# Performance work log

Measured on AMD Instinct MI355X. Metric: run time of the kernel, lower is better.

Reference implementation:

```python
import jax, jax.numpy as jnp
import numpy as np

B, L, C = 8, 3136, 192
HEADS, HEAD_CH = 3, 64
EPS = 1e-5


def _dwconv(x, w, s):
    # depthwise 3x3 conv, SAME padding; w: [3,3,1,C], feature_group_count=C
    return jax.lax.conv_general_dilated(
        x, w, (s, s), 'SAME',
        dimension_numbers=('NHWC', 'HWIO', 'NHWC'),
        feature_group_count=x.shape[-1])


def _proj(x, dw, scale, bias, mean, var, pw, s):
    # depthwise conv -> BN (inference, running stats) -> 1x1 pointwise conv
    h = _dwconv(x, dw, s)
    h = (h - mean) * jax.lax.rsqrt(var + EPS) * scale + bias
    return jax.lax.conv_general_dilated(
        h, pw, (1, 1), 'SAME',
        dimension_numbers=('NHWC', 'HWIO', 'NHWC'))


def setup_inputs() -> dict:
    key = jax.random.key(0)
    ks = jax.random.split(key, 7)
    d = {'x': jax.random.normal(ks[0], (B, L, C), jnp.float32)}
    for i, p in enumerate(['q', 'k', 'v']):
        d[p + '_dw'] = jax.random.normal(ks[i + 1], (3, 3, 1, C), jnp.float32) * 0.1
        d[p + '_scale'] = jnp.ones((C,), jnp.float32)
        d[p + '_bias'] = jnp.zeros((C,), jnp.float32)
        d[p + '_mean'] = jnp.zeros((C,), jnp.float32)
        d[p + '_var'] = jnp.ones((C,), jnp.float32)
        d[p + '_pw'] = jax.random.normal(ks[i + 4], (1, 1, C, HEADS * HEAD_CH), jnp.float32) * 0.05
    d['is_training'] = 0  # inference: BN uses running averages
    return d


def reference(x, q_dw, q_scale, q_bias, q_mean, q_var, q_pw,
              k_dw, k_scale, k_bias, k_mean, k_var, k_pw,
              v_dw, v_scale, v_bias, v_mean, v_var, v_pw,
              is_training):
    S = int(np.ceil(np.sqrt(L)))  # 56; L is a perfect square, so no token padding
    xi = x.reshape(B, S, S, C)
    q = _proj(xi, q_dw, q_scale, q_bias, q_mean, q_var, q_pw, 1)  # [B,56,56,192]
    k = _proj(xi, k_dw, k_scale, k_bias, k_mean, k_var, k_pw, 2)  # [B,28,28,192]
    v = _proj(xi, v_dw, v_scale, v_bias, v_mean, v_var, v_pw, 2)  # [B,28,28,192]
    q = q.reshape(B, -1, HEADS, HEAD_CH) / jnp.sqrt(jnp.float32(HEAD_CH))
    k = k.reshape(B, -1, HEADS, HEAD_CH)
    v = v.reshape(B, -1, HEADS, HEAD_CH)
    attn = jax.nn.softmax(jnp.einsum('bqhd,bkhd->bhqk', q, k), axis=-1)
    o = jnp.einsum('bhqk,bkhd->bqhd', attn, v)
    # num_heads*head_ch == out_ch -> plain head merge, no output projection
    return o.reshape(B, L, HEADS * HEAD_CH)
```

## Files before the change

kernel.cpp:

```cpp
#include <hip/hip_runtime.h>
#include <cmath>

#define EPS_BN 1e-5f

typedef __bf16 bf16;
typedef __bf16 bf16x4 __attribute__((ext_vector_type(4)));
typedef __bf16 bf16x8 __attribute__((ext_vector_type(8)));
typedef float  f32x4  __attribute__((ext_vector_type(4)));

__device__ __forceinline__ void dma16(const bf16* g, bf16* l) {
    __builtin_amdgcn_global_load_lds(
        (const __attribute__((address_space(1))) void*)g,
        (__attribute__((address_space(3))) void*)l, 16, 0, 0);
}

__global__ __launch_bounds__(256) void conv_all_kernel(
    const float* __restrict__ x,
    const float* __restrict__ qdw, const float* __restrict__ qscale,
    const float* __restrict__ qbias, const float* __restrict__ qmean,
    const float* __restrict__ qvar,
    const float* __restrict__ kdw, const float* __restrict__ kscale,
    const float* __restrict__ kbias, const float* __restrict__ kmean,
    const float* __restrict__ kvar,
    const float* __restrict__ vdw, const float* __restrict__ vscale,
    const float* __restrict__ vbias, const float* __restrict__ vmean,
    const float* __restrict__ vvar,
    const float* __restrict__ qpw, const float* __restrict__ kpw,
    const float* __restrict__ vpw,
    bf16* __restrict__ qhi, bf16* __restrict__ qlo,
    bf16* __restrict__ khi, bf16* __restrict__ klo,
    bf16* __restrict__ vhi, bf16* __restrict__ vlo,
    bf16* __restrict__ wt) {
    const int WW = 56, C = 192;
    int bid = blockIdx.x;

    if (bid < 4704) {
        int idx = bid * 256 + threadIdx.x;
        int p  = idx / 48;
        int c4 = (idx - p * 48) * 4;
        int b  = p / 3136;
        int rem = p - b * 3136;
        int oy = rem / 56;
        int ox = rem - oy * 56;
        const float* xb = x + (size_t)b * 3136 * C;

        float4 sc = *(const float4*)&qscale[c4];
        float4 vr = *(const float4*)&qvar[c4];
        float4 bi = *(const float4*)&qbias[c4];
        float4 mn = *(const float4*)&qmean[c4];
        float aA[4] = {sc.x * rsqrtf(vr.x + EPS_BN), sc.y * rsqrtf(vr.y + EPS_BN),
                       sc.z * rsqrtf(vr.z + EPS_BN), sc.w * rsqrtf(vr.w + EPS_BN)};
        float aB[4] = {bi.x - mn.x * aA[0], bi.y - mn.y * aA[1],
                       bi.z - mn.z * aA[2], bi.w - mn.w * aA[3]};
        float s[4] = {0.f, 0.f, 0.f, 0.f};
#pragma unroll
        for (int ky = 0; ky < 3; ky++) {
            int iy = oy + ky - 1;
            bool yok = (iy >= 0) && (iy < 56);
#pragma unroll
            for (int kx = 0; kx < 3; kx++) {
                int ix = ox + kx - 1;
                if (yok && ix >= 0 && ix < WW) {
                    float4 xv = *(const float4*)&xb[((size_t)iy * WW + ix) * C + c4];
                    float4 wv = *(const float4*)&qdw[(ky * 3 + kx) * C + c4];
                    s[0] += xv.x * wv.x; s[1] += xv.y * wv.y;
                    s[2] += xv.z * wv.z; s[3] += xv.w * wv.w;
                }
            }
        }
        bf16x4 hv, lv;
#pragma unroll
        for (int j = 0; j < 4; j++) {
            float av = s[j] * aA[j] + aB[j];
            bf16 hh = (bf16)av;
            hv[j] = hh;
            lv[j] = (bf16)(av - (float)hh);
        }
        *(bf16x4*)&qhi[(size_t)p * C + c4] = hv;
        *(bf16x4*)&qlo[(size_t)p * C + c4] = lv;
    } else if (bid < 5880) {
        int idx = (bid - 4704) * 256 + threadIdx.x;
        int p  = idx / 48;
        int c4 = (idx - p * 48) * 4;
        int b  = p / 784;
        int rem = p - b * 784;
        int oy = rem / 28;
        int ox = rem - oy * 28;
        const float* xb = x + (size_t)b * 3136 * C;

        float ks[4] = {0.f, 0.f, 0.f, 0.f};
        float vs[4] = {0.f, 0.f, 0.f, 0.f};
#pragma unroll
        for (int ky = 0; ky < 3; ky++) {
            int iy = oy * 2 + ky;
            bool yok = iy < 56;
#pragma unroll
            for (int kx = 0; kx < 3; kx++) {
                int ix = ox * 2 + kx;
                if (yok && ix < WW) {
                    float4 xv = *(const float4*)&xb[((size_t)iy * WW + ix) * C + c4];
                    float4 kw = *(const float4*)&kdw[(ky * 3 + kx) * C + c4];
                    float4 vw = *(const float4*)&vdw[(ky * 3 + kx) * C + c4];
                    ks[0] += xv.x * kw.x; ks[1] += xv.y * kw.y;
                    ks[2] += xv.z * kw.z; ks[3] += xv.w * kw.w;
                    vs[0] += xv.x * vw.x; vs[1] += xv.y * vw.y;
                    vs[2] += xv.z * vw.z; vs[3] += xv.w * vw.w;
                }
            }
        }
        float4 ksc = *(const float4*)&kscale[c4];
        float4 kvr = *(const float4*)&kvar[c4];
        float4 kbi = *(const float4*)&kbias[c4];
        float4 kmn = *(const float4*)&kmean[c4];
        float4 vsc = *(const float4*)&vscale[c4];
        float4 vvr = *(const float4*)&vvar[c4];
        float4 vbi = *(const float4*)&vbias[c4];
        float4 vmn = *(const float4*)&vmean[c4];
        float kA[4] = {ksc.x * rsqrtf(kvr.x + EPS_BN), ksc.y * rsqrtf(kvr.y + EPS_BN),
                       ksc.z * rsqrtf(kvr.z + EPS_BN), ksc.w * rsqrtf(kvr.w + EPS_BN)};
        float kB[4] = {kbi.x - kmn.x * kA[0], kbi.y - kmn.y * kA[1],
                       kbi.z - kmn.z * kA[2], kbi.w - kmn.w * kA[3]};
        float vA[4] = {vsc.x * rsqrtf(vvr.x + EPS_BN), vsc.y * rsqrtf(vvr.y + EPS_BN),
                       vsc.z * rsqrtf(vvr.z + EPS_BN), vsc.w * rsqrtf(vvr.w + EPS_BN)};
        float vB[4] = {vbi.x - vmn.x * vA[0], vbi.y - vmn.y * vA[1],
                       vbi.z - vmn.z * vA[2], vbi.w - vmn.w * vA[3]};
        bf16x4 kh, kl, vh, vl;
#pragma unroll
        for (int j = 0; j < 4; j++) {
            float kf = ks[j] * kA[j] + kB[j];
            float vf = vs[j] * vA[j] + vB[j];
            bf16 h1 = (bf16)kf; kh[j] = h1; kl[j] = (bf16)(kf - (float)h1);
            bf16 h2 = (bf16)vf; vh[j] = h2; vl[j] = (bf16)(vf - (float)h2);
        }
        *(bf16x4*)&khi[(size_t)p * C + c4] = kh;
        *(bf16x4*)&klo[(size_t)p * C + c4] = kl;
        *(bf16x4*)&vhi[(size_t)p * C + c4] = vh;
        *(bf16x4*)&vlo[(size_t)p * C + c4] = vl;
    } else {
        int idx = (bid - 5880) * 256 + threadIdx.x;
        if (idx < 3 * 36864) {
            int mat = idx / 36864, r = idx % 36864;
            int n = r / 192, k = r - n * 192;
            const float* src = (mat == 0) ? qpw : (mat == 1) ? kpw : vpw;
            wt[idx] = (bf16)src[k * 192 + n];
        }
    }
}

__global__ __launch_bounds__(256) void gemm_all_kernel(
    const bf16* __restrict__ qhi, const bf16* __restrict__ qlo,
    const bf16* __restrict__ khi, const bf16* __restrict__ klo,
    const bf16* __restrict__ vhi, const bf16* __restrict__ vlo,
    const bf16* __restrict__ wt,
    bf16* __restrict__ qbuf, bf16* __restrict__ kbuf, bf16* __restrict__ vtbuf) {
    __shared__ bf16 Ws[96][200];
    int t = threadIdx.x;
    int bid = blockIdx.x;

    int mode, mt, nh;
    const bf16 *Ahi, *Alo, *Wsrc;
    if (bid < 784)      { mode = 0; mt = bid >> 1;         nh = bid & 1;
                          Ahi = qhi; Alo = qlo; Wsrc = wt; }
    else if (bid < 980) { mode = 1; int r = bid - 784; mt = r >> 1; nh = r & 1;
                          Ahi = khi; Alo = klo; Wsrc = wt + 36864; }
    else                { mode = 2; int r = bid - 980; mt = r >> 1; nh = r & 1;
                          Ahi = vhi; Alo = vlo; Wsrc = wt + 73728; }
    int n0 = nh * 96;

#pragma unroll
    for (int it = 0; it < 9; it++) {
        int idx = it * 256 + t;
        int n = idx / 24, ck = idx - n * 24;
        *(uint4*)&Ws[n][ck * 8] = *(const uint4*)&Wsrc[(size_t)(n0 + n) * 192 + ck * 8];
    }
    __syncthreads();

    int lane = t & 63, wid = t >> 6;
    int l16 = lane & 15, quad = lane >> 4;
    int wrow = wid * 16;
    int m0 = mt * 64;

    f32x4 acc[6];
#pragma unroll
    for (int n = 0; n < 6; n++) acc[n] = f32x4{0.f, 0.f, 0.f, 0.f};

    const bf16* arh = Ahi + (size_t)(m0 + wrow + l16) * 192;
    const bf16* arl = Alo + (size_t)(m0 + wrow + l16) * 192;
#pragma unroll
    for (int kc = 0; kc < 6; kc++) {
        bf16x8 ah = *(const bf16x8*)(arh + kc * 32 + quad * 8);
        bf16x8 al = *(const bf16x8*)(arl + kc * 32 + quad * 8);
#pragma unroll
        for (int n = 0; n < 6; n++) {
            bf16x8 bfr = *(const bf16x8*)&Ws[n * 16 + l16][kc * 32 + quad * 8];
            acc[n] = __builtin_amdgcn_mfma_f32_16x16x32_bf16(al, bfr, acc[n], 0, 0, 0);
            acc[n] = __builtin_amdgcn_mfma_f32_16x16x32_bf16(ah, bfr, acc[n], 0, 0, 0);
        }
    }

    if (mode == 2) {
#pragma unroll
        for (int reg = 0; reg < 4; reg++) {
            int row = m0 + wrow + quad * 4 + reg;
            int b = row / 784;
            int loc = row - b * 784;
#pragma unroll
            for (int n = 0; n < 6; n++) {
                int col = n0 + n * 16 + l16;
                int h = col >> 6, d = col & 63;
                vtbuf[(((size_t)b * 3 + h) * 64 + d) * 784 + loc] = (bf16)acc[n][reg];
            }
        }
    } else {
        bf16* outp = (mode == 0) ? qbuf : kbuf;
        const float s = (mode == 0) ? 0.125f : 1.0f;
#pragma unroll
        for (int reg = 0; reg < 4; reg++) {
            size_t row = m0 + wrow + quad * 4 + reg;
#pragma unroll
            for (int n = 0; n < 6; n++)
                outp[row * 192 + n0 + n * 16 + l16] = (bf16)(acc[n][reg] * s);
        }
    }
}

__global__ __launch_bounds__(256)
__attribute__((amdgpu_waves_per_eu(3, 3)))
void attn3_kernel(const bf16* __restrict__ qb,
                  const bf16* __restrict__ kb,
                  const bf16* __restrict__ vtb,
                  float* __restrict__ out) {
    const int LQ = 3136, LK = 784, C = 192;
    int qt = blockIdx.x, h = blockIdx.y, b = blockIdx.z;

    __shared__ bf16 Ks[2][7168];
    __shared__ bf16 Vts[8192];
    __shared__ bf16 Ps[4096];

    int t    = threadIdx.x;
    int lane = t & 63;
    int wid  = t >> 6;
    int l16  = lane & 15;
    int quad = lane >> 4;
    int wrow = wid * 16;
    int l7   = l16 & 7;
    int qh   = quad >> 1;

    const bf16* kbase  = kb + (size_t)b * LK * C + h * 64;
    const bf16* vtbase = vtb + ((size_t)(b * 3 + h)) * 64 * LK;

    const bf16* ksrc = kbase + (lane >> 3) * C + (((lane & 7) ^ (lane >> 3)) * 8);

    int voff[4];
#pragma unroll
    for (int i = 0; i < 4; i++) {
        int s = wid + 4 * i;
        int j = s * 64 + lane;
        int row = j >> 4;
        int l = (j & 15) ^ (row & 7);
        voff[i] = row * LK + l * 8;
    }

    for (int s = wid; s < 14; s += 4)
        dma16(ksrc + s * 8 * C, &Ks[0][s * 512]);

    bf16x8 qfrag[2];
    {
        const bf16* qrow = qb + ((size_t)b * LQ + qt * 64 + wrow + l16) * C + h * 64;
        qfrag[0] = *(const bf16x8*)(qrow + quad * 8);
        qfrag[1] = *(const bf16x8*)(qrow + 32 + quad * 8);
    }

    int kA0 = l16 * 64 + (((quad    ) ^ l7) * 8);
    int kA1 = l16 * 64 + (((quad + 4) ^ l7) * 8);

    int prow   = (wrow + l16) * 64;
    int pwbase = prow + (quad & 1) * 4;

    float m_run = -INFINITY, l_run = 0.f;
    f32x4 o_acc[4];
#pragma unroll
    for (int dt = 0; dt < 4; dt++) o_acc[dt] = f32x4{0.f, 0.f, 0.f, 0.f};

    __syncthreads();

    for (int c = 0; c < 7; c++) {
        const int cur = c & 1, nxt = cur ^ 1;
        const int j0 = c * 112;

#pragma unroll
        for (int i = 0; i < 4; i++)
            dma16(vtbase + j0 + voff[i], Vts + (wid + 4 * i) * 512);
        __builtin_amdgcn_sched_barrier(0);

        if (c < 6) {
            const bf16* kn = ksrc + (size_t)(c + 1) * 112 * C;
            for (int s = wid; s < 14; s += 4)
                dma16(kn + s * 8 * C, &Ks[nxt][s * 512]);
        }
        __builtin_amdgcn_sched_barrier(0);

        f32x4 st[7];
#pragma unroll
        for (int kb7 = 0; kb7 < 7; kb7++) st[kb7] = f32x4{0.f, 0.f, 0.f, 0.f};
#pragma unroll
        for (int kk = 0; kk < 2; kk++) {
            int kA = (kk == 0) ? kA0 : kA1;
#pragma unroll
            for (int kb7 = 0; kb7 < 7; kb7++) {
                bf16x8 afrag = *(const bf16x8*)&Ks[cur][kb7 * 1024 + kA];
                st[kb7] = __builtin_amdgcn_mfma_f32_16x16x32_bf16(afrag, qfrag[kk], st[kb7], 0, 0, 0);
            }
        }

        float mx = -INFINITY;
#pragma unroll
        for (int kb7 = 0; kb7 < 7; kb7++)
#pragma unroll
            for (int r = 0; r < 4; r++) mx = fmaxf(mx, st[kb7][r]);
        mx = fmaxf(mx, __shfl_xor(mx, 16, 64));
        mx = fmaxf(mx, __shfl_xor(mx, 32, 64));
        float m_new = fmaxf(m_run, mx);
        float alpha = __expf(m_run - m_new);

        float rs = 0.f;
        bf16x4 pk[7];
#pragma unroll
        for (int kb7 = 0; kb7 < 7; kb7++) {
            bf16x4 pv;
#pragma unroll
            for (int r = 0; r < 4; r++) {
                float p = __expf(st[kb7][r] - m_new);
                rs += p;
                pv[r] = (bf16)p;
            }
            pk[kb7] = pv;
        }
        rs += __shfl_xor(rs, 16, 64);
        rs += __shfl_xor(rs, 32, 64);
        l_run = l_run * alpha + rs;
        m_run = m_new;
#pragma unroll
        for (int dt = 0; dt < 4; dt++)
#pragma unroll
            for (int r = 0; r < 4; r++) o_acc[dt][r] *= alpha;

#pragma unroll
        for (int kb = 0; kb < 4; kb++)
            *(bf16x4*)&Ps[pwbase + (((kb * 2 + qh) ^ l7) * 8)] = pk[kb];

        if (c < 6) {
            if (wid < 2) asm volatile("s_waitcnt vmcnt(4)" ::: "memory");
            else         asm volatile("s_waitcnt vmcnt(3)" ::: "memory");
        } else {
            asm volatile("s_waitcnt vmcnt(0)" ::: "memory");
        }
        __builtin_amdgcn_s_barrier();
        __builtin_amdgcn_sched_barrier(0);

#pragma unroll
        for (int kk = 0; kk < 2; kk++) {
            bf16x8 pfrag = *(const bf16x8*)&Ps[prow + (((kk * 4 + quad) ^ l7) * 8)];
#pragma unroll
            for (int dt = 0; dt < 4; dt++) {
                bf16x8 vfrag = *(const bf16x8*)&Vts[(dt * 16 + l16) * 128
                                                   + (((kk * 4 + quad) ^ l7) * 8)];
                o_acc[dt] = __builtin_amdgcn_mfma_f32_16x16x32_bf16(vfrag, pfrag, o_acc[dt], 0, 0, 0);
            }
        }

#pragma unroll
        for (int kb = 0; kb < 3; kb++)
            *(bf16x4*)&Ps[pwbase + (((kb * 2 + qh) ^ l7) * 8)] = pk[4 + kb];
        {
            bf16x4 zv = {(bf16)0.f, (bf16)0.f, (bf16)0.f, (bf16)0.f};
            *(bf16x4*)&Ps[pwbase + (((6 + qh) ^ l7) * 8)] = zv;
        }

#pragma unroll
        for (int kk = 2; kk < 4; kk++) {
            bf16x8 pfrag = *(const bf16x8*)&Ps[prow + ((((kk - 2) * 4 + quad) ^ l7) * 8)];
#pragma unroll
            for (int dt = 0; dt < 4; dt++) {
                bf16x8 vfrag = *(const bf16x8*)&Vts[(dt * 16 + l16) * 128
                                                   + (((kk * 4 + quad) ^ l7) * 8)];
                o_acc[dt] = __builtin_amdgcn_mfma_f32_16x16x32_bf16(vfrag, pfrag, o_acc[dt], 0, 0, 0);
            }
        }

        __syncthreads();
    }

    float invl = 1.f / l_run;
    float* ob = out + ((size_t)b * LQ + qt * 64 + wrow + l16) * C + h * 64;
#pragma unroll
    for (int dt = 0; dt < 4; dt++) {
        float4 v4 = {o_acc[dt][0] * invl, o_acc[dt][1] * invl,
                     o_acc[dt][2] * invl, o_acc[dt][3] * invl};
        *(float4*)(ob + dt * 16 + quad * 4) = v4;
    }
}

extern "C" void kernel_launch(void* const* d_in, const int* in_sizes, int n_in,
                              void* d_out, int out_size, void* d_ws, size_t ws_size,
                              hipStream_t stream) {
    const float* x = (const float*)d_in[0];

    const float* q_dw = (const float*)d_in[1];
    const float* q_scale = (const float*)d_in[2];
    const float* q_bias = (const float*)d_in[3];
    const float* q_mean = (const float*)d_in[4];
    const float* q_var = (const float*)d_in[5];
    const float* q_pw = (const float*)d_in[6];

    const float* k_dw = (const float*)d_in[7];
    const float* k_scale = (const float*)d_in[8];
    const float* k_bias = (const float*)d_in[9];
    const float* k_mean = (const float*)d_in[10];
    const float* k_var = (const float*)d_in[11];
    const float* k_pw = (const float*)d_in[12];

    const float* v_dw = (const float*)d_in[13];
    const float* v_scale = (const float*)d_in[14];
    const float* v_bias = (const float*)d_in[15];
    const float* v_mean = (const float*)d_in[16];
    const float* v_var = (const float*)d_in[17];
    const float* v_pw = (const float*)d_in[18];

    float* out = (float*)d_out;

    char* ws = (char*)d_ws;
    bf16* qhi = (bf16*)(ws);
    bf16* qlo = (bf16*)(ws + 9633792);
    bf16* khi = (bf16*)(ws + 19267584);
    bf16* klo = (bf16*)(ws + 21676032);
    bf16* vhi = (bf16*)(ws + 24084480);
    bf16* vlo = (bf16*)(ws + 26492928);
    bf16* qbuf = (bf16*)(ws + 28901376);
    bf16* kbuf = (bf16*)(ws + 38535168);
    bf16* vtbuf = (bf16*)(ws + 40943616);
    bf16* wt = (bf16*)(ws + 43352064);

    conv_all_kernel<<<6312, 256, 0, stream>>>(
        x,
        q_dw, q_scale, q_bias, q_mean, q_var,
        k_dw, k_scale, k_bias, k_mean, k_var,
        v_dw, v_scale, v_bias, v_mean, v_var,
        q_pw, k_pw, v_pw,
        qhi, qlo, khi, klo, vhi, vlo, wt);

    gemm_all_kernel<<<1176, 256, 0, stream>>>(
        qhi, qlo, khi, klo, vhi, vlo, wt, qbuf, kbuf, vtbuf);

    attn3_kernel<<<dim3(49, 3, 8), 256, 0, stream>>>(qbuf, kbuf, vtbuf, out);
}
```

Measured before the change: 176.6 us.

## Fold log2e into Q scale, use hardware exp2, defer softmax rescale, transpose V epilogue

Folds log2(e) into the query scale so the attention softmax can use the native v_exp_f32 (exp2) instruction instead of __expf. It also skips the running-max update and accumulator rescale when the new block max stays within a threshold of the current max, cutting per-tile exp and multiply work. The V projection swaps the MFMA operands so each lane holds consecutive output rows, which gives more contiguous transposed stores into the V^T buffer. The deferred rescale lets unnormalized probabilities reach 2^8, which could lose some bf16 precision.

```diff
diff --git a/kernel.cpp b/kernel.cpp
--- a/kernel.cpp
+++ b/kernel.cpp
@@ -12,6 +12,12 @@
     __builtin_amdgcn_global_load_lds(
         (const __attribute__((address_space(1))) void*)g,
         (__attribute__((address_space(3))) void*)l, 16, 0, 0);
+}
+
+__device__ __forceinline__ float exp2_hw(float x) {
+    float r;
+    asm("v_exp_f32 %0, %1" : "=v"(r) : "v"(x));
+    return r;
 }
 
 __global__ __launch_bounds__(256) void conv_all_kernel(
@@ -186,34 +192,45 @@
 
     const bf16* arh = Ahi + (size_t)(m0 + wrow + l16) * 192;
     const bf16* arl = Alo + (size_t)(m0 + wrow + l16) * 192;
-#pragma unroll
-    for (int kc = 0; kc < 6; kc++) {
-        bf16x8 ah = *(const bf16x8*)(arh + kc * 32 + quad * 8);
-        bf16x8 al = *(const bf16x8*)(arl + kc * 32 + quad * 8);
-#pragma unroll
-        for (int n = 0; n < 6; n++) {
-            bf16x8 bfr = *(const bf16x8*)&Ws[n * 16 + l16][kc * 32 + quad * 8];
-            acc[n] = __builtin_amdgcn_mfma_f32_16x16x32_bf16(al, bfr, acc[n], 0, 0, 0);
-            acc[n] = __builtin_amdgcn_mfma_f32_16x16x32_bf16(ah, bfr, acc[n], 0, 0, 0);
-        }
-    }
 
     if (mode == 2) {
 #pragma unroll
-        for (int reg = 0; reg < 4; reg++) {
-            int row = m0 + wrow + quad * 4 + reg;
-            int b = row / 784;
-            int loc = row - b * 784;
+        for (int kc = 0; kc < 6; kc++) {
+            bf16x8 ah = *(const bf16x8*)(arh + kc * 32 + quad * 8);
+            bf16x8 al = *(const bf16x8*)(arl + kc * 32 + quad * 8);
 #pragma unroll
             for (int n = 0; n < 6; n++) {
-                int col = n0 + n * 16 + l16;
-                int h = col >> 6, d = col & 63;
-                vtbuf[(((size_t)b * 3 + h) * 64 + d) * 784 + loc] = (bf16)acc[n][reg];
-            }
-        }
+                bf16x8 bfr = *(const bf16x8*)&Ws[n * 16 + l16][kc * 32 + quad * 8];
+                acc[n] = __builtin_amdgcn_mfma_f32_16x16x32_bf16(bfr, al, acc[n], 0, 0, 0);
+                acc[n] = __builtin_amdgcn_mfma_f32_16x16x32_bf16(bfr, ah, acc[n], 0, 0, 0);
+            }
+        }
+        int row = m0 + wrow + l16;
+        int bb  = row / 784;
+        int loc = row - bb * 784;
+        bf16* vbase = vtbuf + (size_t)bb * 3 * 64 * 784 + loc;
+#pragma unroll
+        for (int n = 0; n < 6; n++)
+#pragma unroll
+            for (int reg = 0; reg < 4; reg++) {
+                int col = n0 + n * 16 + quad * 4 + reg;
+                int hh = col >> 6, d = col & 63;
+                vbase[((size_t)hh * 64 + d) * 784] = (bf16)acc[n][reg];
+            }
     } else {
+#pragma unroll
+        for (int kc = 0; kc < 6; kc++) {
+            bf16x8 ah = *(const bf16x8*)(arh + kc * 32 + quad * 8);
+            bf16x8 al = *(const bf16x8*)(arl + kc * 32 + quad * 8);
+#pragma unroll
+            for (int n = 0; n < 6; n++) {
+                bf16x8 bfr = *(const bf16x8*)&Ws[n * 16 + l16][kc * 32 + quad * 8];
+                acc[n] = __builtin_amdgcn_mfma_f32_16x16x32_bf16(al, bfr, acc[n], 0, 0, 0);
+                acc[n] = __builtin_amdgcn_mfma_f32_16x16x32_bf16(ah, bfr, acc[n], 0, 0, 0);
+            }
+        }
         bf16* outp = (mode == 0) ? qbuf : kbuf;
-        const float s = (mode == 0) ? 0.125f : 1.0f;
+        const float s = (mode == 0) ? 0.18033688f : 1.0f;
 #pragma unroll
         for (int reg = 0; reg < 4; reg++) {
             size_t row = m0 + wrow + quad * 4 + reg;
@@ -320,8 +337,9 @@
             for (int r = 0; r < 4; r++) mx = fmaxf(mx, st[kb7][r]);
         mx = fmaxf(mx, __shfl_xor(mx, 16, 64));
         mx = fmaxf(mx, __shfl_xor(mx, 32, 64));
-        float m_new = fmaxf(m_run, mx);
-        float alpha = __expf(m_run - m_new);
+
+        bool defer = __all(mx - m_run <= 8.0f);
+        float m_new = defer ? m_run : fmaxf(m_run, mx);
 
         float rs = 0.f;
         bf16x4 pk[7];
@@ -330,7 +348,7 @@
             bf16x4 pv;
 #pragma unroll
             for (int r = 0; r < 4; r++) {
-                float p = __expf(st[kb7][r] - m_new);
+                float p = exp2_hw(st[kb7][r] - m_new);
                 rs += p;
                 pv[r] = (bf16)p;
             }
@@ -338,12 +356,17 @@
         }
         rs += __shfl_xor(rs, 16, 64);
         rs += __shfl_xor(rs, 32, 64);
-        l_run = l_run * alpha + rs;
-        m_run = m_new;
-#pragma unroll
-        for (int dt = 0; dt < 4; dt++)
-#pragma unroll
-            for (int r = 0; r < 4; r++) o_acc[dt][r] *= alpha;
+        if (defer) {
+            l_run += rs;
+        } else {
+            float alpha = exp2_hw(m_run - m_new);
+            l_run = l_run * alpha + rs;
+            m_run = m_new;
+#pragma unroll
+            for (int dt = 0; dt < 4; dt++)
+#pragma unroll
+                for (int r = 0; r < 4; r++) o_acc[dt][r] *= alpha;
+        }
 
 #pragma unroll
         for (int kb = 0; kb < 4; kb++)
```

Measured after the change: 174.5 us. Within noise of the previous version (-1.2%).
